# Optimization experiments

Measured on AMD Instinct MI355X. Metric: run time of the kernel, lower is better.

Reference implementation:

```python
import jax, jax.numpy as jnp
import numpy as np

M = 5  # neighbours per down point (M_i = 5 when n_up > 5)


def _per_graph(h, s_l, scores, W_emb, b_emb):
    # h: [N,H], s_l: [N,3], scores: [N]
    N, H = h.shape
    n_up = N // 4  # floor(0.25 * N)
    top_idx = jnp.argsort(-scores)[:n_up]
    up_mask = jnp.zeros((N,), bool).at[top_idx].set(True)
    up_idx = jnp.sort(top_idx)                     # up nodes in ascending node order
    down_idx = jnp.argsort(up_mask)[: N - n_up]    # stable: down nodes ascending

    # embedding_features_to_att: Linear(H+4 -> H) on concat(h, s_l, scores)
    feat = jnp.concatenate([h, s_l, scores[:, None]], axis=1) @ W_emb + b_emb  # [N,H]

    # directional KNN: for each down point, M nearest up points in 3D coords
    d2 = jnp.sum((s_l[down_idx][:, None, :] - s_l[up_idx][None, :, :]) ** 2, -1)  # [Nd,Nu]
    _, nn_local = jax.lax.top_k(-d2, M)            # [Nd,M] indices into up set
    dst = up_idx[nn_local].reshape(-1)             # edge destinations (up nodes)
    src = jnp.repeat(down_idx, M)                  # edge sources (down nodes)

    # DGL update_all: copy src 'features' -> max reduce at dst; no-msg nodes = 0
    msgs = feat[src]                               # [Nd*M, H]
    out = jnp.full((N, H), -jnp.inf, feat.dtype).at[dst].max(msgs)
    out = jnp.where(jnp.isneginf(out), jnp.zeros((), feat.dtype), out)
    return out, up_mask


def setup_inputs() -> dict:
    key = jax.random.key(0)
    k1, k2, k3, k4, k5 = jax.random.split(key, 5)
    B, N, H = 8, 8192, 256
    return {
        "h": jax.random.normal(k1, (B, N, H), jnp.float32),
        "s_l": jax.random.normal(k2, (B, N, 3), jnp.float32),
        "scores": jax.random.uniform(k3, (B, N), jnp.float32),
        "W_emb": jax.random.normal(k4, (H + 4, H), jnp.float32) * 0.02,
        "b_emb": jax.random.normal(k5, (H,), jnp.float32) * 0.02,
    }


def reference(h, s_l, scores, W_emb, b_emb):
    out, up_mask = jax.vmap(_per_graph, in_axes=(0, 0, 0, None, None))(
        h, s_l, scores, W_emb, b_emb)
    B, N, H = out.shape
    return out.reshape(B * N, H), up_mask.reshape(-1)
```

## Files before the change

kernel.cpp:

```cpp
#include <hip/hip_runtime.h>

#define Bb 8
#define Nn 8192
#define Hh 256
#define NUP 2048
#define NDOWN (Nn - NUP)
#define MM 5
#define EPB (NDOWN * MM)
#define KP 288
#define LDA 36
#define LSTW 17

typedef short v8s __attribute__((ext_vector_type(8)));
typedef float v4f __attribute__((ext_vector_type(4)));

#define INFKEY 0x7F800000FFFFFFFFull

__device__ __forceinline__ unsigned short bfc(float f) {
    unsigned u = __float_as_uint(f);
    return (unsigned short)((u + 0x7FFFu + ((u >> 16) & 1u)) >> 16);
}

template <int NB>
__device__ void find_kth_bin(const int* hist, int kth, int tid,
                             int* wsumA, int* res, int* out_bin, int* out_cntgt) {
    constexpr int PER = NB / 1024;
    int ln = tid & 63, wv = tid >> 6;
    int b0 = NB - 1 - PER * tid;
    int c0 = hist[b0];
    int c1 = (PER == 2) ? hist[b0 - 1] : 0;
    int tot = c0 + c1;
    int x = tot;
    #pragma unroll
    for (int off = 1; off < 64; off <<= 1) {
        int y = __shfl_up(x, off);
        if (ln >= off) x += y;
    }
    if (ln == 63) wsumA[wv] = x;
    __syncthreads();
    int wbase = 0;
    for (int w = 0; w < wv; w++) wbase += wsumA[w];
    int excl = wbase + x - tot;
    if (excl < kth && excl + c0 >= kth) { res[0] = b0; res[1] = excl; }
    else if (PER == 2 && excl + c0 < kth && excl + c0 + c1 >= kth) { res[0] = b0 - 1; res[1] = excl + c0; }
    __syncthreads();
    *out_bin = res[0];
    *out_cntgt = res[1];
}

__global__ __launch_bounds__(1024) void select_kernel(
        const float* __restrict__ scores, const float* __restrict__ sl,
        int* __restrict__ mask, float4* __restrict__ upc,
        float4* __restrict__ dnc, int* __restrict__ up_local,
        int* __restrict__ deg) {
    int b = blockIdx.x;
    int tid = threadIdx.x;
    int ln = tid & 63, wv = tid >> 6;
    __shared__ int hist[2048];
    __shared__ int wsumA[16], wsumB[16];
    __shared__ int res[2];
    __shared__ int sbase[2];
    const float* s = scores + (size_t)b * Nn;

    deg[b * NUP + tid] = 0;
    deg[b * NUP + 1024 + tid] = 0;

    hist[tid] = 0; hist[tid + 1024] = 0;
    __syncthreads();
    for (int t = tid; t < Nn; t += 1024)
        atomicAdd(&hist[__float_as_uint(s[t]) >> 21], 1);
    __syncthreads();
    int B1, gt1;
    find_kth_bin<2048>(hist, NUP, tid, wsumA, res, &B1, &gt1);
    int slots1 = NUP - gt1;

    hist[tid] = 0; hist[tid + 1024] = 0;
    __syncthreads();
    for (int t = tid; t < Nn; t += 1024) {
        unsigned u = __float_as_uint(s[t]);
        if ((int)(u >> 21) == B1) atomicAdd(&hist[(u >> 10) & 0x7FF], 1);
    }
    __syncthreads();
    int B2, gt2;
    find_kth_bin<2048>(hist, slots1, tid, wsumA, res, &B2, &gt2);
    int slots2 = slots1 - gt2;
    unsigned hi22 = ((unsigned)B1 << 11) | (unsigned)B2;

    hist[tid] = 0; hist[tid + 1024] = 0;
    __syncthreads();
    for (int t = tid; t < Nn; t += 1024) {
        unsigned u = __float_as_uint(s[t]);
        if ((u >> 10) == hi22) atomicAdd(&hist[u & 0x3FF], 1);
    }
    __syncthreads();
    int B3, gt3;
    find_kth_bin<1024>(hist, slots2, tid, wsumA, res, &B3, &gt3);
    int slots_eq = slots2 - gt3;
    unsigned T = (hi22 << 10) | (unsigned)B3;

    if (tid == 0) { sbase[0] = 0; sbase[1] = 0; }
    __syncthreads();
    for (int t0 = 0; t0 < Nn; t0 += 1024) {
        int node = t0 + tid;
        int g = b * Nn + node;
        unsigned u = __float_as_uint(s[node]);
        bool eq = (u == T);
        unsigned long long bal = __ballot(eq);
        unsigned long long lmask = (1ull << ln) - 1ull;
        int pre = __popcll(bal & lmask);
        if (ln == 0) wsumA[wv] = __popcll(bal);
        __syncthreads();
        int eqbase = sbase[0];
        for (int w = 0; w < wv; w++) eqbase += wsumA[w];
        bool up = (u > T) || (eq && (eqbase + pre) < slots_eq);
        unsigned long long bal2 = __ballot(up);
        int pre2 = __popcll(bal2 & lmask);
        if (ln == 0) wsumB[wv] = __popcll(bal2);
        __syncthreads();
        int upbase = sbase[1];
        for (int w = 0; w < wv; w++) upbase += wsumB[w];
        float4 c;
        c.x = sl[(size_t)g * 3 + 0];
        c.y = sl[(size_t)g * 3 + 1];
        c.z = sl[(size_t)g * 3 + 2];
        c.w = __int_as_float(node);
        if (up) {
            upc[b * NUP + upbase + pre2] = c;
            up_local[g] = upbase + pre2;
        } else {
            dnc[b * NDOWN + node - (upbase + pre2)] = c;
        }
        mask[g] = up ? 1 : 0;
        __syncthreads();
        if (tid == 0) {
            int se = 0, su = 0;
            for (int w = 0; w < 16; w++) { se += wsumA[w]; su += wsumB[w]; }
            sbase[0] += se; sbase[1] += su;
        }
        __syncthreads();
    }
}

__global__ __launch_bounds__(512) void knn_brute(
        const float4* __restrict__ upc, const float4* __restrict__ dnc,
        const int* __restrict__ up_local, int* __restrict__ knn,
        int* __restrict__ deg) {
    int b = blockIdx.y;
    int tid = threadIdx.x;
    int sub = tid >> 6, dn = tid & 63;
    __shared__ float4 stage[NUP];
    __shared__ float sThr[8 * MM * 64];
    __shared__ unsigned long long lst[64 * LSTW];
    __shared__ int lcnt[64];

    float4 d = dnc[b * NDOWN + blockIdx.x * 64 + dn];
    float xd = d.x, yd = d.y, zd = d.z;
    int node = __float_as_int(d.w);

    const float4* U = upc + b * NUP;
    #pragma unroll
    for (int q = 0; q < 4; q++) stage[q * 512 + tid] = U[q * 512 + tid];
    if (tid < 64) lcnt[tid] = 0;
    __syncthreads();

    float L[MM];
    #pragma unroll
    for (int m = 0; m < MM; m++) L[m] = 3.4e38f;
    const int j0 = sub * 256;
    #pragma unroll 4
    for (int j = j0; j < j0 + 256; ++j) {
        float4 c = stage[j];
        float dx = c.x - xd, dy = c.y - yd, dz = c.z - zd;
        float d2 = fmaf(dx, dx, fmaf(dy, dy, dz * dz));
        #pragma unroll
        for (int m = 0; m < MM; m++) {
            float lo = fminf(d2, L[m]), hi = fmaxf(d2, L[m]);
            L[m] = lo; d2 = hi;
        }
    }
    #pragma unroll
    for (int m = 0; m < MM; m++) sThr[(sub * MM + m) * 64 + dn] = L[m];
    __syncthreads();

    if (sub == 0) {
        float F[MM];
        #pragma unroll
        for (int m = 0; m < MM; m++) F[m] = 3.4e38f;
        for (int l = 0; l < 8; l++) {
            #pragma unroll
            for (int m = 0; m < MM; m++) {
                float v = sThr[(l * MM + m) * 64 + dn];
                #pragma unroll
                for (int k = 0; k < MM; k++) {
                    float lo = fminf(v, F[k]), hi = fmaxf(v, F[k]);
                    F[k] = lo; v = hi;
                }
            }
        }
        sThr[dn] = F[MM - 1];
    }
    __syncthreads();
    float thr = sThr[dn];

    #pragma unroll 4
    for (int j = j0; j < j0 + 256; ++j) {
        float4 c = stage[j];
        float dx = c.x - xd, dy = c.y - yd, dz = c.z - zd;
        float d2 = fmaf(dx, dx, fmaf(dy, dy, dz * dz));
        if (d2 <= thr) {
            unsigned long long key =
                ((unsigned long long)__float_as_uint(d2) << 32) |
                (unsigned long long)(unsigned)__float_as_int(c.w);
            int s = atomicAdd(&lcnt[dn], 1);
            if (s < LSTW - 1) lst[dn * LSTW + s] = key;
        }
    }
    __syncthreads();

    if (sub == 0) {
        unsigned long long fin[MM];
        #pragma unroll
        for (int m = 0; m < MM; m++) fin[m] = 0xFFFFFFFFFFFFFFFFull;
        int n = min(lcnt[dn], LSTW - 1);
        for (int s = 0; s < n; s++) {
            unsigned long long cand = lst[dn * LSTW + s];
            #pragma unroll
            for (int m = 0; m < MM; m++) {
                bool lt = cand < fin[m];
                unsigned long long lo = lt ? cand : fin[m];
                unsigned long long hi = lt ? fin[m] : cand;
                fin[m] = lo; cand = hi;
            }
        }
        int g = b * Nn + node;
        #pragma unroll
        for (int m = 0; m < MM; m++) {
            int nid = (int)(unsigned)(fin[m] & 0xFFFFFFFFull);
            knn[g * MM + m] = nid;
            atomicAdd(&deg[b * NUP + up_local[b * Nn + nid]], 1);
        }
    }
}

__global__ void wt_kernel(const float* __restrict__ W, const float* __restrict__ bias,
                          unsigned short* __restrict__ Wt) {
    int n = blockIdx.x;
    int k = threadIdx.x;
    Wt[n * KP + k] = bfc(W[(size_t)k * Hh + n]);
    if (k < KP - 256) {
        int kk = 256 + k;
        unsigned short v = 0;
        if (kk < 260)       v = bfc(W[(size_t)kk * Hh + n]);
        else if (kk == 260) v = bfc(bias[n]);
        Wt[n * KP + kk] = v;
    }
}

__global__ void feat_mfma(const float* __restrict__ h, const float* __restrict__ sl,
                          const float* __restrict__ sc, const unsigned short* __restrict__ Wt,
                          float* __restrict__ out) {
    int b = blockIdx.z;
    int m0 = blockIdx.x * 128;
    int n0 = blockIdx.y * 128;
    int tid = threadIdx.x;
    __shared__ unsigned short Al[128 * LDA];
    __shared__ unsigned short Bl[128 * LDA];
    int wid = tid >> 6, lane = tid & 63;
    int wm = (wid & 1) * 64, wn = (wid >> 1) * 64;
    int lm = lane & 15, quad = lane >> 4;
    v4f acc[4][4];
    #pragma unroll
    for (int i = 0; i < 4; i++)
        #pragma unroll
        for (int j = 0; j < 4; j++)
            acc[i][j] = (v4f){0.f, 0.f, 0.f, 0.f};
    const float* Ab = h + ((size_t)b * Nn + m0) * Hh;
    for (int t = 0; t < 9; t++) {
        int k0 = t * 32;
        __syncthreads();
        if (t < 8) {
            #pragma unroll
            for (int q = 0; q < 4; q++) {
                int e = q * 256 + tid;
                int row = e >> 3, kq = e & 7;
                float4 v = *(const float4*)(Ab + (size_t)row * Hh + k0 + kq * 4);
                ushort4 o = make_ushort4(bfc(v.x), bfc(v.y), bfc(v.z), bfc(v.w));
                *(ushort4*)(Al + row * LDA + kq * 4) = o;
            }
        } else if (tid < 128) {
            int row = tid;
            int g = b * Nn + m0 + row;
            unsigned short r[32];
            #pragma unroll
            for (int k = 0; k < 32; k++) r[k] = 0;
            r[0] = bfc(sl[(size_t)g * 3 + 0]);
            r[1] = bfc(sl[(size_t)g * 3 + 1]);
            r[2] = bfc(sl[(size_t)g * 3 + 2]);
            r[3] = bfc(sc[g]);
            r[4] = 0x3F80;
            #pragma unroll
            for (int q = 0; q < 8; q++)
                *(ushort4*)(Al + row * LDA + q * 4) =
                    make_ushort4(r[q * 4], r[q * 4 + 1], r[q * 4 + 2], r[q * 4 + 3]);
        }
        #pragma unroll
        for (int q = 0; q < 4; q++) {
            int e = q * 256 + tid;
            int n = e >> 3, kq = e & 7;
            ushort4 v = *(const ushort4*)(Wt + (size_t)(n0 + n) * KP + k0 + kq * 4);
            *(ushort4*)(Bl + n * LDA + kq * 4) = v;
        }
        __syncthreads();
        v8s af[4], bfr[4];
        #pragma unroll
        for (int i = 0; i < 4; i++)
            af[i] = *(const v8s*)(Al + (wm + i * 16 + lm) * LDA + quad * 8);
        #pragma unroll
        for (int j = 0; j < 4; j++)
            bfr[j] = *(const v8s*)(Bl + (wn + j * 16 + lm) * LDA + quad * 8);
        #pragma unroll
        for (int i = 0; i < 4; i++)
            #pragma unroll
            for (int j = 0; j < 4; j++)
                acc[i][j] = __builtin_amdgcn_mfma_f32_16x16x32_bf16(af[i], bfr[j], acc[i][j], 0, 0, 0);
    }
    #pragma unroll
    for (int i = 0; i < 4; i++) {
        #pragma unroll
        for (int r = 0; r < 4; r++) {
            int row = m0 + wm + i * 16 + quad * 4 + r;
            size_t base = ((size_t)b * Nn + row) * Hh + n0 + wn + lm;
            #pragma unroll
            for (int j = 0; j < 4; j++)
                out[base + j * 16] = acc[i][j][r];
        }
    }
}

__global__ __launch_bounds__(1024) void csr_scan(const int* __restrict__ deg,
                                                 int* __restrict__ rowptr,
                                                 int* __restrict__ cursor) {
    int b = blockIdx.x;
    int tid = threadIdx.x;
    int ln = tid & 63, wv = tid >> 6;
    __shared__ int wsum[16];
    int d0 = deg[b * NUP + 2 * tid], d1 = deg[b * NUP + 2 * tid + 1];
    int s = d0 + d1;
    int x = s;
    #pragma unroll
    for (int off = 1; off < 64; off <<= 1) {
        int y = __shfl_up(x, off);
        if (ln >= off) x += y;
    }
    if (ln == 63) wsum[wv] = x;
    __syncthreads();
    int base = 0;
    for (int w = 0; w < wv; w++) base += wsum[w];
    int excl = base + x - s;
    rowptr[b * (NUP + 1) + 2 * tid] = excl;
    rowptr[b * (NUP + 1) + 2 * tid + 1] = excl + d0;
    cursor[b * NUP + 2 * tid] = excl;
    cursor[b * NUP + 2 * tid + 1] = excl + d0;
    if (tid == 1023) rowptr[b * (NUP + 1) + NUP] = excl + s;
}

__global__ void csr_fill(const int* __restrict__ mask, const int* __restrict__ knn,
                         const int* __restrict__ up_local, int* __restrict__ cursor,
                         int* __restrict__ edges) {
    int b = blockIdx.y;
    int i = blockIdx.x * 256 + threadIdx.x;
    int g = b * Nn + i;
    if (mask[g]) return;
    #pragma unroll
    for (int m = 0; m < MM; m++) {
        int un = knn[g * MM + m];
        int slot = atomicAdd(&cursor[b * NUP + up_local[b * Nn + un]], 1);
        edges[b * EPB + slot] = i;
    }
}

__global__ void gather_kernel(const float4* __restrict__ upc, const int* __restrict__ rowptr,
                              const int* __restrict__ edges, float* __restrict__ out) {
    int b = blockIdx.y;
    int u = blockIdx.x * 4 + (threadIdx.x >> 6);
    int lane = threadIdx.x & 63;
    int node = __float_as_int(upc[b * NUP + u].w);
    int start = rowptr[b * (NUP + 1) + u];
    int end   = rowptr[b * (NUP + 1) + u + 1];
    const int* eb = edges + b * EPB;
    size_t rowbase = (size_t)b * Nn * Hh + (size_t)(lane << 2);
    float4 a0 = make_float4(-3.4e38f, -3.4e38f, -3.4e38f, -3.4e38f);
    float4 a1 = a0;
    int e = start;
    for (; e + 2 <= end; e += 2) {
        int s0 = eb[e], s1 = eb[e + 1];
        float4 v0 = *(const float4*)(out + rowbase + (size_t)s0 * Hh);
        float4 v1 = *(const float4*)(out + rowbase + (size_t)s1 * Hh);
        a0.x = fmaxf(a0.x, v0.x); a0.y = fmaxf(a0.y, v0.y);
        a0.z = fmaxf(a0.z, v0.z); a0.w = fmaxf(a0.w, v0.w);
        a1.x = fmaxf(a1.x, v1.x); a1.y = fmaxf(a1.y, v1.y);
        a1.z = fmaxf(a1.z, v1.z); a1.w = fmaxf(a1.w, v1.w);
    }
    if (e < end) {
        int s0 = eb[e];
        float4 v0 = *(const float4*)(out + rowbase + (size_t)s0 * Hh);
        a0.x = fmaxf(a0.x, v0.x); a0.y = fmaxf(a0.y, v0.y);
        a0.z = fmaxf(a0.z, v0.z); a0.w = fmaxf(a0.w, v0.w);
    }
    float4 r;
    r.x = fmaxf(a0.x, a1.x); r.y = fmaxf(a0.y, a1.y);
    r.z = fmaxf(a0.z, a1.z); r.w = fmaxf(a0.w, a1.w);
    if (start == end) r = make_float4(0.f, 0.f, 0.f, 0.f);
    *(float4*)(out + rowbase + (size_t)node * Hh) = r;
}

__global__ void finalize_kernel(const int* __restrict__ mask, float* __restrict__ out) {
    int b = blockIdx.y;
    int node = blockIdx.x * 4 + (threadIdx.x >> 6);
    int g = b * Nn + node;
    int lane = threadIdx.x & 63;
    bool up = mask[g] != 0;
    if (!up)
        *(float4*)(out + (size_t)g * Hh + (lane << 2)) = make_float4(0.f, 0.f, 0.f, 0.f);
    if (lane == 0) out[(size_t)Bb * Nn * Hh + g] = up ? 1.0f : 0.0f;
}

extern "C" void kernel_launch(void* const* d_in, const int* in_sizes, int n_in,
                              void* d_out, int out_size, void* d_ws, size_t ws_size,
                              hipStream_t stream) {
    const float* h    = (const float*)d_in[0];
    const float* sl   = (const float*)d_in[1];
    const float* sc   = (const float*)d_in[2];
    const float* W    = (const float*)d_in[3];
    const float* bias = (const float*)d_in[4];

    char* ws = (char*)d_ws;
    int* mask = (int*)ws;                 ws += (size_t)Bb * Nn * sizeof(int);
    int* knn  = (int*)ws;                 ws += (size_t)Bb * Nn * MM * sizeof(int);
    float4* upc = (float4*)ws;            ws += (size_t)Bb * NUP * sizeof(float4);
    float4* dnc = (float4*)ws;            ws += (size_t)Bb * NDOWN * sizeof(float4);
    unsigned short* Wt = (unsigned short*)ws; ws += (size_t)Hh * KP * sizeof(unsigned short);
    int* up_local = (int*)ws;             ws += (size_t)Bb * Nn * sizeof(int);
    int* deg = (int*)ws;                  ws += (size_t)Bb * NUP * sizeof(int);
    int* cursor = (int*)ws;               ws += (size_t)Bb * NUP * sizeof(int);
    int* rowptr = (int*)ws;               ws += (size_t)Bb * (NUP + 1) * sizeof(int);
    int* edges = (int*)ws;
    float* outf = (float*)d_out;

    dim3 blk(256);
    select_kernel<<<dim3(Bb), dim3(1024), 0, stream>>>(sc, sl, mask, upc, dnc,
                                                       up_local, deg);
    knn_brute<<<dim3(NDOWN / 64, Bb), dim3(512), 0, stream>>>(upc, dnc,
                                                              up_local, knn, deg);
    csr_scan<<<dim3(Bb), dim3(1024), 0, stream>>>(deg, rowptr, cursor);
    csr_fill<<<dim3(Nn / 256, Bb), blk, 0, stream>>>(mask, knn, up_local, cursor, edges);
    wt_kernel<<<dim3(Hh), blk, 0, stream>>>(W, bias, Wt);
    feat_mfma<<<dim3(Nn / 128, 2, Bb), blk, 0, stream>>>(h, sl, sc, Wt, outf);
    gather_kernel<<<dim3(NUP / 4, Bb), blk, 0, stream>>>(upc, rowptr, edges, outf);
    finalize_kernel<<<dim3(Nn / 4, Bb), blk, 0, stream>>>(mask, outf);
}
```

Before: 300.8 us.

## Compute features only for down nodes and use local up indices in KNN

The feature GEMM now runs only over down nodes, gathering their rows through the down-node id list, because only down-node features are ever read as messages. That removes a quarter of the matmul work and output writes. KNN now stores up-set local indices directly, so the up_local map and its indirect lookups go away, and the staged coordinates move to a struct-of-arrays layout in LDS. The gather loop is unrolled to four independent accumulators for more memory-level parallelism. The cost is gathered, non-contiguous row loads and stores in the GEMM.

```diff
diff --git a/kernel.cpp b/kernel.cpp
--- a/kernel.cpp
+++ b/kernel.cpp
@@ -14,8 +14,6 @@
 typedef short v8s __attribute__((ext_vector_type(8)));
 typedef float v4f __attribute__((ext_vector_type(4)));
 
-#define INFKEY 0x7F800000FFFFFFFFull
-
 __device__ __forceinline__ unsigned short bfc(float f) {
     unsigned u = __float_as_uint(f);
     return (unsigned short)((u + 0x7FFFu + ((u >> 16) & 1u)) >> 16);
@@ -51,8 +49,7 @@
 __global__ __launch_bounds__(1024) void select_kernel(
         const float* __restrict__ scores, const float* __restrict__ sl,
         int* __restrict__ mask, float4* __restrict__ upc,
-        float4* __restrict__ dnc, int* __restrict__ up_local,
-        int* __restrict__ deg) {
+        float4* __restrict__ dnc, int* __restrict__ deg) {
     int b = blockIdx.x;
     int tid = threadIdx.x;
     int ln = tid & 63, wv = tid >> 6;
@@ -126,7 +123,6 @@
         c.w = __int_as_float(node);
         if (up) {
             upc[b * NUP + upbase + pre2] = c;
-            up_local[g] = upbase + pre2;
         } else {
             dnc[b * NDOWN + node - (upbase + pre2)] = c;
         }
@@ -143,15 +139,15 @@
 
 __global__ __launch_bounds__(512) void knn_brute(
         const float4* __restrict__ upc, const float4* __restrict__ dnc,
-        const int* __restrict__ up_local, int* __restrict__ knn,
-        int* __restrict__ deg) {
+        int* __restrict__ knn, int* __restrict__ deg) {
     int b = blockIdx.y;
     int tid = threadIdx.x;
     int sub = tid >> 6, dn = tid & 63;
-    __shared__ float4 stage[NUP];
-    __shared__ float sThr[8 * MM * 64];
-    __shared__ unsigned long long lst[64 * LSTW];
+    __shared__ float xs[NUP], ys[NUP], zs[NUP];
+    __shared__ unsigned long long Ubuf[1312];
     __shared__ int lcnt[64];
+    float* sF = (float*)Ubuf;
+    unsigned long long* lst = Ubuf + 32;
 
     float4 d = dnc[b * NDOWN + blockIdx.x * 64 + dn];
     float xd = d.x, yd = d.y, zd = d.z;
@@ -159,7 +155,11 @@
 
     const float4* U = upc + b * NUP;
     #pragma unroll
-    for (int q = 0; q < 4; q++) stage[q * 512 + tid] = U[q * 512 + tid];
+    for (int q = 0; q < 4; q++) {
+        int i = q * 512 + tid;
+        float4 u = U[i];
+        xs[i] = u.x; ys[i] = u.y; zs[i] = u.z;
+    }
     if (tid < 64) lcnt[tid] = 0;
     __syncthreads();
 
@@ -169,8 +169,7 @@
     const int j0 = sub * 256;
     #pragma unroll 4
     for (int j = j0; j < j0 + 256; ++j) {
-        float4 c = stage[j];
-        float dx = c.x - xd, dy = c.y - yd, dz = c.z - zd;
+        float dx = xs[j] - xd, dy = ys[j] - yd, dz = zs[j] - zd;
         float d2 = fmaf(dx, dx, fmaf(dy, dy, dz * dz));
         #pragma unroll
         for (int m = 0; m < MM; m++) {
@@ -179,7 +178,7 @@
         }
     }
     #pragma unroll
-    for (int m = 0; m < MM; m++) sThr[(sub * MM + m) * 64 + dn] = L[m];
+    for (int m = 0; m < MM; m++) sF[(sub * MM + m) * 64 + dn] = L[m];
     __syncthreads();
 
     if (sub == 0) {
@@ -189,7 +188,7 @@
         for (int l = 0; l < 8; l++) {
             #pragma unroll
             for (int m = 0; m < MM; m++) {
-                float v = sThr[(l * MM + m) * 64 + dn];
+                float v = sF[(l * MM + m) * 64 + dn];
                 #pragma unroll
                 for (int k = 0; k < MM; k++) {
                     float lo = fminf(v, F[k]), hi = fmaxf(v, F[k]);
@@ -197,20 +196,19 @@
                 }
             }
         }
-        sThr[dn] = F[MM - 1];
-    }
-    __syncthreads();
-    float thr = sThr[dn];
+        sF[dn] = F[MM - 1];
+    }
+    __syncthreads();
+    float thr = sF[dn];
 
     #pragma unroll 4
     for (int j = j0; j < j0 + 256; ++j) {
-        float4 c = stage[j];
-        float dx = c.x - xd, dy = c.y - yd, dz = c.z - zd;
+        float dx = xs[j] - xd, dy = ys[j] - yd, dz = zs[j] - zd;
         float d2 = fmaf(dx, dx, fmaf(dy, dy, dz * dz));
         if (d2 <= thr) {
             unsigned long long key =
                 ((unsigned long long)__float_as_uint(d2) << 32) |
-                (unsigned long long)(unsigned)__float_as_int(c.w);
+                (unsigned long long)(unsigned)j;
             int s = atomicAdd(&lcnt[dn], 1);
             if (s < LSTW - 1) lst[dn * LSTW + s] = key;
         }
@@ -235,9 +233,9 @@
         int g = b * Nn + node;
         #pragma unroll
         for (int m = 0; m < MM; m++) {
-            int nid = (int)(unsigned)(fin[m] & 0xFFFFFFFFull);
-            knn[g * MM + m] = nid;
-            atomicAdd(&deg[b * NUP + up_local[b * Nn + nid]], 1);
+            int lid = (int)(unsigned)(fin[m] & 0xFFFFFFFFull);
+            knn[g * MM + m] = lid;
+            atomicAdd(&deg[b * NUP + lid], 1);
         }
     }
 }
@@ -258,23 +256,25 @@
 
 __global__ void feat_mfma(const float* __restrict__ h, const float* __restrict__ sl,
                           const float* __restrict__ sc, const unsigned short* __restrict__ Wt,
-                          float* __restrict__ out) {
+                          const float4* __restrict__ dnc, float* __restrict__ out) {
     int b = blockIdx.z;
     int m0 = blockIdx.x * 128;
     int n0 = blockIdx.y * 128;
     int tid = threadIdx.x;
     __shared__ unsigned short Al[128 * LDA];
     __shared__ unsigned short Bl[128 * LDA];
+    __shared__ int ndid[128];
     int wid = tid >> 6, lane = tid & 63;
     int wm = (wid & 1) * 64, wn = (wid >> 1) * 64;
     int lm = lane & 15, quad = lane >> 4;
+    if (tid < 128) ndid[tid] = __float_as_int(dnc[b * NDOWN + m0 + tid].w);
     v4f acc[4][4];
     #pragma unroll
     for (int i = 0; i < 4; i++)
         #pragma unroll
         for (int j = 0; j < 4; j++)
             acc[i][j] = (v4f){0.f, 0.f, 0.f, 0.f};
-    const float* Ab = h + ((size_t)b * Nn + m0) * Hh;
+    const float* hb = h + (size_t)b * Nn * Hh;
     for (int t = 0; t < 9; t++) {
         int k0 = t * 32;
         __syncthreads();
@@ -283,13 +283,13 @@
             for (int q = 0; q < 4; q++) {
                 int e = q * 256 + tid;
                 int row = e >> 3, kq = e & 7;
-                float4 v = *(const float4*)(Ab + (size_t)row * Hh + k0 + kq * 4);
+                float4 v = *(const float4*)(hb + (size_t)ndid[row] * Hh + k0 + kq * 4);
                 ushort4 o = make_ushort4(bfc(v.x), bfc(v.y), bfc(v.z), bfc(v.w));
                 *(ushort4*)(Al + row * LDA + kq * 4) = o;
             }
         } else if (tid < 128) {
             int row = tid;
-            int g = b * Nn + m0 + row;
+            int g = b * Nn + ndid[row];
             unsigned short r[32];
             #pragma unroll
             for (int k = 0; k < 32; k++) r[k] = 0;
@@ -328,8 +328,8 @@
     for (int i = 0; i < 4; i++) {
         #pragma unroll
         for (int r = 0; r < 4; r++) {
-            int row = m0 + wm + i * 16 + quad * 4 + r;
-            size_t base = ((size_t)b * Nn + row) * Hh + n0 + wn + lm;
+            int lrow = wm + i * 16 + quad * 4 + r;
+            size_t base = ((size_t)b * Nn + ndid[lrow]) * Hh + n0 + wn + lm;
             #pragma unroll
             for (int j = 0; j < 4; j++)
                 out[base + j * 16] = acc[i][j][r];
@@ -365,8 +365,7 @@
 }
 
 __global__ void csr_fill(const int* __restrict__ mask, const int* __restrict__ knn,
-                         const int* __restrict__ up_local, int* __restrict__ cursor,
-                         int* __restrict__ edges) {
+                         int* __restrict__ cursor, int* __restrict__ edges) {
     int b = blockIdx.y;
     int i = blockIdx.x * 256 + threadIdx.x;
     int g = b * Nn + i;
@@ -374,7 +373,7 @@
     #pragma unroll
     for (int m = 0; m < MM; m++) {
         int un = knn[g * MM + m];
-        int slot = atomicAdd(&cursor[b * NUP + up_local[b * Nn + un]], 1);
+        int slot = atomicAdd(&cursor[b * NUP + un], 1);
         edges[b * EPB + slot] = i;
     }
 }
@@ -390,26 +389,34 @@
     const int* eb = edges + b * EPB;
     size_t rowbase = (size_t)b * Nn * Hh + (size_t)(lane << 2);
     float4 a0 = make_float4(-3.4e38f, -3.4e38f, -3.4e38f, -3.4e38f);
-    float4 a1 = a0;
+    float4 a1 = a0, a2 = a0, a3 = a0;
     int e = start;
-    for (; e + 2 <= end; e += 2) {
-        int s0 = eb[e], s1 = eb[e + 1];
+    for (; e + 4 <= end; e += 4) {
+        int s0 = eb[e], s1 = eb[e + 1], s2 = eb[e + 2], s3 = eb[e + 3];
         float4 v0 = *(const float4*)(out + rowbase + (size_t)s0 * Hh);
         float4 v1 = *(const float4*)(out + rowbase + (size_t)s1 * Hh);
+        float4 v2 = *(const float4*)(out + rowbase + (size_t)s2 * Hh);
+        float4 v3 = *(const float4*)(out + rowbase + (size_t)s3 * Hh);
         a0.x = fmaxf(a0.x, v0.x); a0.y = fmaxf(a0.y, v0.y);
         a0.z = fmaxf(a0.z, v0.z); a0.w = fmaxf(a0.w, v0.w);
         a1.x = fmaxf(a1.x, v1.x); a1.y = fmaxf(a1.y, v1.y);
         a1.z = fmaxf(a1.z, v1.z); a1.w = fmaxf(a1.w, v1.w);
-    }
-    if (e < end) {
+        a2.x = fmaxf(a2.x, v2.x); a2.y = fmaxf(a2.y, v2.y);
+        a2.z = fmaxf(a2.z, v2.z); a2.w = fmaxf(a2.w, v2.w);
+        a3.x = fmaxf(a3.x, v3.x); a3.y = fmaxf(a3.y, v3.y);
+        a3.z = fmaxf(a3.z, v3.z); a3.w = fmaxf(a3.w, v3.w);
+    }
+    for (; e < end; e++) {
         int s0 = eb[e];
         float4 v0 = *(const float4*)(out + rowbase + (size_t)s0 * Hh);
         a0.x = fmaxf(a0.x, v0.x); a0.y = fmaxf(a0.y, v0.y);
         a0.z = fmaxf(a0.z, v0.z); a0.w = fmaxf(a0.w, v0.w);
     }
     float4 r;
-    r.x = fmaxf(a0.x, a1.x); r.y = fmaxf(a0.y, a1.y);
-    r.z = fmaxf(a0.z, a1.z); r.w = fmaxf(a0.w, a1.w);
+    r.x = fmaxf(fmaxf(a0.x, a1.x), fmaxf(a2.x, a3.x));
+    r.y = fmaxf(fmaxf(a0.y, a1.y), fmaxf(a2.y, a3.y));
+    r.z = fmaxf(fmaxf(a0.z, a1.z), fmaxf(a2.z, a3.z));
+    r.w = fmaxf(fmaxf(a0.w, a1.w), fmaxf(a2.w, a3.w));
     if (start == end) r = make_float4(0.f, 0.f, 0.f, 0.f);
     *(float4*)(out + rowbase + (size_t)node * Hh) = r;
 }
@@ -440,7 +447,6 @@
     float4* upc = (float4*)ws;            ws += (size_t)Bb * NUP * sizeof(float4);
     float4* dnc = (float4*)ws;            ws += (size_t)Bb * NDOWN * sizeof(float4);
     unsigned short* Wt = (unsigned short*)ws; ws += (size_t)Hh * KP * sizeof(unsigned short);
-    int* up_local = (int*)ws;             ws += (size_t)Bb * Nn * sizeof(int);
     int* deg = (int*)ws;                  ws += (size_t)Bb * NUP * sizeof(int);
     int* cursor = (int*)ws;               ws += (size_t)Bb * NUP * sizeof(int);
     int* rowptr = (int*)ws;               ws += (size_t)Bb * (NUP + 1) * sizeof(int);
@@ -448,14 +454,12 @@
     float* outf = (float*)d_out;
 
     dim3 blk(256);
-    select_kernel<<<dim3(Bb), dim3(1024), 0, stream>>>(sc, sl, mask, upc, dnc,
-                                                       up_local, deg);
-    knn_brute<<<dim3(NDOWN / 64, Bb), dim3(512), 0, stream>>>(upc, dnc,
-                                                              up_local, knn, deg);
+    select_kernel<<<dim3(Bb), dim3(1024), 0, stream>>>(sc, sl, mask, upc, dnc, deg);
+    knn_brute<<<dim3(NDOWN / 64, Bb), dim3(512), 0, stream>>>(upc, dnc, knn, deg);
     csr_scan<<<dim3(Bb), dim3(1024), 0, stream>>>(deg, rowptr, cursor);
-    csr_fill<<<dim3(Nn / 256, Bb), blk, 0, stream>>>(mask, knn, up_local, cursor, edges);
+    csr_fill<<<dim3(Nn / 256, Bb), blk, 0, stream>>>(mask, knn, cursor, edges);
     wt_kernel<<<dim3(Hh), blk, 0, stream>>>(W, bias, Wt);
-    feat_mfma<<<dim3(Nn / 128, 2, Bb), blk, 0, stream>>>(h, sl, sc, Wt, outf);
+    feat_mfma<<<dim3(NDOWN / 128, 2, Bb), blk, 0, stream>>>(h, sl, sc, Wt, dnc, outf);
     gather_kernel<<<dim3(NUP / 4, Bb), blk, 0, stream>>>(upc, rowptr, edges, outf);
     finalize_kernel<<<dim3(Nn / 4, Bb), blk, 0, stream>>>(mask, outf);
 }
```

Result: faster. 278.9 us (-7.3%).
